# Kernel tuning notes

Hardware: AMD Instinct MI355X
Metric: run time of the kernel (lower is better)

The kernel has to match this reference:

```python
import jax, jax.numpy as jnp
import numpy as np

ALPHA = 0.2     # LeakyReLU negative slope
NEG = -1e9      # mask value for non-edges (matches -1000000000)
N, S, O, H, E = 8192, 128, 64, 4, 262144


def setup_inputs() -> dict:
    key = jax.random.key(0)
    ks = jax.random.split(key, 6)
    x = jax.random.normal(ks[0], (1, N, S), jnp.float32)
    edges = jax.random.randint(ks[1], (2, E), 0, N, dtype=jnp.int64)
    values = jnp.ones((E,), jnp.float32)
    # xavier_normal with gain=1.414
    W_heads = jax.random.normal(ks[2], (H, S, O), jnp.float32) * (1.414 * np.sqrt(2.0 / (S + O)))
    a_heads = jax.random.normal(ks[3], (H, 2 * O), jnp.float32) * (1.414 * np.sqrt(2.0 / (1 + 2 * O)))
    lin_w = jax.random.normal(ks[4], (1, H), jnp.float32) * 0.5
    lin_b = jnp.zeros((1,), jnp.float32)
    return {"x": x, "edges": edges, "values": values, "W_heads": W_heads,
            "a_heads": a_heads, "lin_w": lin_w, "lin_b": lin_b}


def reference(x, edges, values, W_heads, a_heads, lin_w, lin_b):
    b, n, s = x.shape
    Ntot = b * n
    xf = x.reshape(Ntot, s)
    # per-head projection: [H, N, O]
    h = jnp.einsum('ns,hso->hno', xf, W_heads)
    e0, e1 = edges[0], edges[1]
    Od = h.shape[-1]
    # per-edge attention logits for all heads: a . [h_src || h_dst], shape [H, E]
    atts = (jnp.einsum('heo,ho->he', h[:, e0, :], a_heads[:, :Od])
            + jnp.einsum('heo,ho->he', h[:, e1, :], a_heads[:, Od:]))
    atts = jax.nn.leaky_relu(atts, negative_slope=ALPHA)
    # combine heads with a 1-output linear: [E]
    mt = (atts.T @ lin_w.T + lin_b)[:, 0]
    new_values = values * mt
    # scatter to dense NxN (duplicate edges sum, like sparse coo to_dense)
    dense = jnp.zeros((Ntot, Ntot), x.dtype).at[e0, e1].add(new_values)
    a_dense = jnp.zeros((Ntot, Ntot), values.dtype).at[e0, e1].add(values)
    mask = jnp.where(a_dense == 0, NEG, jnp.where(a_dense == 1, 0.0, a_dense))
    # softmax over dim 0, as in the original
    return jax.nn.softmax(dense + mask, axis=0)
```

## Files before the change

kernel.cpp:

```cpp
#include <hip/hip_runtime.h>
#include <math.h>


#define ALPHA 0.2f
constexpr int S = 128;
constexpr int O = 64;
constexpr int H = 4;
constexpr int CAP = 128;
constexpr int RPB = 4;

__global__ void __launch_bounds__(256) k1_scores(
    const float* __restrict__ x, const float* __restrict__ W, const float* __restrict__ a,
    float4* __restrict__ s_src4, float4* __restrict__ s_dst4,
    int* __restrict__ col_cursor, int* __restrict__ row_cursor, int* __restrict__ empty_cnt,
    int N)
{
    __shared__ float wsbuf[2 * H * S];
    int tid = threadIdx.x;
    for (int t = tid; t < 2 * H * S; t += 256) {
        int which = t / (H * S);
        int hs = t % (H * S);
        int h = hs / S, s = hs % S;
        const float* Wr = W + ((size_t)h * S + s) * O;
        const float* av = a + h * 2 * O + which * O;
        float acc = 0.f;
        for (int o = 0; o < O; ++o) acc += Wr[o] * av[o];
        wsbuf[t] = acc;
    }
    __syncthreads();
    int n = blockIdx.x * 256 + tid;
    if (n == 0) empty_cnt[0] = 0;
    if (n >= N) return;
    col_cursor[n] = 0;
    row_cursor[n] = 0;
    const float* wsrc = wsbuf;
    const float* wdst = wsbuf + H * S;
    const float4* xr = (const float4*)(x + (size_t)n * S);
    float accs[H] = {0, 0, 0, 0}, accd[H] = {0, 0, 0, 0};
    for (int i = 0; i < S / 4; ++i) {
        float4 v = xr[i];
#pragma unroll
        for (int h = 0; h < H; ++h) {
            const float* p = wsrc + h * S + i * 4;
            const float* q = wdst + h * S + i * 4;
            accs[h] += v.x * p[0] + v.y * p[1] + v.z * p[2] + v.w * p[3];
            accd[h] += v.x * q[0] + v.y * q[1] + v.z * q[2] + v.w * q[3];
        }
    }
    s_src4[n] = make_float4(accs[0], accs[1], accs[2], accs[3]);
    s_dst4[n] = make_float4(accd[0], accd[1], accd[2], accd[3]);
}

__global__ void __launch_bounds__(256) k2_scatter(
    const int* __restrict__ edges, const float* __restrict__ values,
    const float4* __restrict__ s_src4, const float4* __restrict__ s_dst4,
    const float* __restrict__ lin_w, const float* __restrict__ lin_b,
    int* __restrict__ col_cursor, int* __restrict__ row_cursor,
    int4* __restrict__ col_ent, int* __restrict__ col_r, int N, int E)
{
    int e = blockIdx.x * 256 + threadIdx.x;
    if (e >= E) return;
    int r = edges[e];
    int c = edges[(size_t)E + e];
    if ((unsigned)r >= (unsigned)N || (unsigned)c >= (unsigned)N) return;
    float4 ss = s_src4[r];
    float4 sd = s_dst4[c];
    float att0 = ss.x + sd.x, att1 = ss.y + sd.y, att2 = ss.z + sd.z, att3 = ss.w + sd.w;
    att0 = att0 >= 0.f ? att0 : ALPHA * att0;
    att1 = att1 >= 0.f ? att1 : ALPHA * att1;
    att2 = att2 >= 0.f ? att2 : ALPHA * att2;
    att3 = att3 >= 0.f ? att3 : ALPHA * att3;
    float mt = lin_b[0] + att0 * lin_w[0] + att1 * lin_w[1] + att2 * lin_w[2] + att3 * lin_w[3];
    float av = values[e];
    float nv = av * mt;
    int posc = atomicAdd(&col_cursor[c], 1);
    int posr = atomicAdd(&row_cursor[r], 1);
    if (posc < CAP && posr < CAP) {
        int4 ent;
        ent.x = r;
        ent.y = __float_as_int(nv);
        ent.z = __float_as_int(av);
        ent.w = r * CAP + posr;
        col_ent[(size_t)c * CAP + posc] = ent;
        col_r[(size_t)r * CAP + posr] = c;
    }
}

__global__ void __launch_bounds__(256) k3_softmax(
    const int4* __restrict__ col_ent, const int* __restrict__ col_cursor,
    float* __restrict__ val_r, int* __restrict__ empty_list, int* __restrict__ empty_cnt,
    int N)
{
    int wave = threadIdx.x >> 6, lane = threadIdx.x & 63;
    int j = blockIdx.x * 4 + wave;
    if (j >= N) return;
    int m = col_cursor[j];
    if (m > CAP) m = CAP;
    if (m == 0) {
        if (lane == 0) { int p = atomicAdd(empty_cnt, 1); empty_list[p] = j; }
        return;
    }
    const int4* base = col_ent + (size_t)j * CAP;
    if (m <= 64) {
        bool mine = lane < m;
        int r; float v, av; int link = 0;
        if (mine) {
            int4 ent = base[lane];
            r = ent.x; v = __int_as_float(ent.y); av = __int_as_float(ent.z); link = ent.w;
        } else {
            r = -1 - lane; v = 0.f; av = 0.f;
        }
        float dsum = 0.f, asum = 0.f;
        bool first = true;
        for (int l = 0; l < 64; ++l) {
            int rl = __shfl(r, l);
            float vl = __shfl(v, l);
            float al = __shfl(av, l);
            if (rl == r) {
                dsum += vl; asum += al;
                if (l < lane) first = false;
            }
        }
        float mask = (asum == 1.0f) ? 0.f : asum;
        float val = dsum + mask;
        float lmax = (mine && first) ? val : -INFINITY;
#pragma unroll
        for (int off = 32; off; off >>= 1) lmax = fmaxf(lmax, __shfl_xor(lmax, off));
        float ex = (mine && first) ? expf(val - lmax) : 0.f;
        float lsum = ex;
#pragma unroll
        for (int off = 32; off; off >>= 1) lsum += __shfl_xor(lsum, off);
        float inv = 1.0f / lsum;
        if (mine) val_r[link] = expf(val - lmax) * inv;
    } else {
        float lmax = -INFINITY;
        for (int k = lane; k < m; k += 64) {
            int rk = base[k].x;
            bool first = true;
            float ds = 0.f, as = 0.f;
            for (int l = 0; l < m; ++l) {
                int4 el = base[l];
                if (el.x == rk) {
                    if (l < k) first = false;
                    ds += __int_as_float(el.y);
                    as += __int_as_float(el.z);
                }
            }
            if (first) {
                float mk = (as == 1.0f) ? 0.f : as;
                lmax = fmaxf(lmax, ds + mk);
            }
        }
#pragma unroll
        for (int off = 32; off; off >>= 1) lmax = fmaxf(lmax, __shfl_xor(lmax, off));
        float lsum = 0.f;
        for (int k = lane; k < m; k += 64) {
            int rk = base[k].x;
            bool first = true;
            float ds = 0.f, as = 0.f;
            for (int l = 0; l < m; ++l) {
                int4 el = base[l];
                if (el.x == rk) {
                    if (l < k) first = false;
                    ds += __int_as_float(el.y);
                    as += __int_as_float(el.z);
                }
            }
            if (first) {
                float mk = (as == 1.0f) ? 0.f : as;
                lsum += expf(ds + mk - lmax);
            }
        }
#pragma unroll
        for (int off = 32; off; off >>= 1) lsum += __shfl_xor(lsum, off);
        float inv = 1.0f / lsum;
        for (int k = lane; k < m; k += 64) {
            int rk = base[k].x;
            float ds = 0.f, as = 0.f;
            for (int l = 0; l < m; ++l) {
                int4 el = base[l];
                if (el.x == rk) {
                    ds += __int_as_float(el.y);
                    as += __int_as_float(el.z);
                }
            }
            float mk = (as == 1.0f) ? 0.f : as;
            val_r[base[k].w] = expf(ds + mk - lmax) * inv;
        }
    }
}

__global__ void __launch_bounds__(256) k4_rowwrite(
    const int* __restrict__ col_r, const float* __restrict__ val_r,
    const int* __restrict__ row_cursor, const int* __restrict__ empty_list,
    const int* __restrict__ empty_cnt, float* __restrict__ out, int N)
{
    int t = threadIdx.x;
    const float4 z4 = make_float4(0.f, 0.f, 0.f, 0.f);
    int ec = empty_cnt[0];
    float u = 1.0f / (float)N;
    int n4 = N / 4;
#pragma unroll
    for (int q = 0; q < RPB; ++q) {
        int i = blockIdx.x * RPB + q;
        if (i >= N) return;
        float* orow = out + (size_t)i * N;
        float4* o4 = (float4*)orow;
        for (int k = t; k < n4; k += 256) o4[k] = z4;
        __syncthreads();
        int mr = row_cursor[i];
        if (mr > CAP) mr = CAP;
        const int* cr = col_r + (size_t)i * CAP;
        const float* vr = val_r + (size_t)i * CAP;
        for (int k = t; k < mr; k += 256) orow[cr[k]] = vr[k];
        for (int k = t; k < ec; k += 256) orow[empty_list[k]] = u;
    }
}

extern "C" void kernel_launch(void* const* d_in, const int* in_sizes, int n_in,
                              void* d_out, int out_size, void* d_ws, size_t ws_size,
                              hipStream_t stream) {
    const float* x = (const float*)d_in[0];
    const int* edges = (const int*)d_in[1];
    const float* values = (const float*)d_in[2];
    const float* W = (const float*)d_in[3];
    const float* a = (const float*)d_in[4];
    const float* lin_w = (const float*)d_in[5];
    const float* lin_b = (const float*)d_in[6];
    float* out = (float*)d_out;

    int N = in_sizes[0] / S;
    int E = in_sizes[2];

    char* wsb = (char*)d_ws;
    size_t off = 0;
    auto alloc = [&](size_t bytes) -> void* {
        void* p = wsb + off;
        off += (bytes + 255) & ~(size_t)255;
        return p;
    };
    float4* s_src4 = (float4*)alloc((size_t)N * 16);
    float4* s_dst4 = (float4*)alloc((size_t)N * 16);
    int* col_cursor = (int*)alloc((size_t)N * 4);
    int* row_cursor = (int*)alloc((size_t)N * 4);
    int* empty_cnt = (int*)alloc(256);
    int* empty_list = (int*)alloc((size_t)N * 4);
    int4* col_ent = (int4*)alloc((size_t)N * CAP * 16);
    int* col_r = (int*)alloc((size_t)N * CAP * 4);
    float* val_r = (float*)alloc((size_t)N * CAP * 4);

    k1_scores<<<(N + 255) / 256, 256, 0, stream>>>(x, W, a, s_src4, s_dst4,
                                                   col_cursor, row_cursor, empty_cnt, N);
    k2_scatter<<<(E + 255) / 256, 256, 0, stream>>>(edges, values, s_src4, s_dst4, lin_w, lin_b,
                                                    col_cursor, row_cursor, col_ent, col_r, N, E);
    k3_softmax<<<(N + 3) / 4, 256, 0, stream>>>(col_ent, col_cursor, val_r,
                                                empty_list, empty_cnt, N);
    k4_rowwrite<<<(N + RPB - 1) / RPB, 256, 0, stream>>>(col_r, val_r, row_cursor,
                                                         empty_list, empty_cnt, out, N);
}
```

Baseline: 121.0 us.

## Fuse output zeroing into score kernel and scatter softmax directly to output

```diff
diff --git a/kernel.cpp b/kernel.cpp
--- a/kernel.cpp
+++ b/kernel.cpp
@@ -7,56 +7,61 @@
 constexpr int O = 64;
 constexpr int H = 4;
 constexpr int CAP = 128;
-constexpr int RPB = 4;
-
-__global__ void __launch_bounds__(256) k1_scores(
+
+__global__ void __launch_bounds__(256) k1_zero_scores(
     const float* __restrict__ x, const float* __restrict__ W, const float* __restrict__ a,
     float4* __restrict__ s_src4, float4* __restrict__ s_dst4,
-    int* __restrict__ col_cursor, int* __restrict__ row_cursor, int* __restrict__ empty_cnt,
-    int N)
+    int* __restrict__ col_cursor, float4* __restrict__ out4,
+    int N, size_t n4tot)
 {
     __shared__ float wsbuf[2 * H * S];
     int tid = threadIdx.x;
-    for (int t = tid; t < 2 * H * S; t += 256) {
-        int which = t / (H * S);
-        int hs = t % (H * S);
-        int h = hs / S, s = hs % S;
-        const float* Wr = W + ((size_t)h * S + s) * O;
-        const float* av = a + h * 2 * O + which * O;
-        float acc = 0.f;
-        for (int o = 0; o < O; ++o) acc += Wr[o] * av[o];
-        wsbuf[t] = acc;
-    }
-    __syncthreads();
-    int n = blockIdx.x * 256 + tid;
-    if (n == 0) empty_cnt[0] = 0;
-    if (n >= N) return;
-    col_cursor[n] = 0;
-    row_cursor[n] = 0;
-    const float* wsrc = wsbuf;
-    const float* wdst = wsbuf + H * S;
-    const float4* xr = (const float4*)(x + (size_t)n * S);
-    float accs[H] = {0, 0, 0, 0}, accd[H] = {0, 0, 0, 0};
-    for (int i = 0; i < S / 4; ++i) {
-        float4 v = xr[i];
-#pragma unroll
-        for (int h = 0; h < H; ++h) {
-            const float* p = wsrc + h * S + i * 4;
-            const float* q = wdst + h * S + i * 4;
-            accs[h] += v.x * p[0] + v.y * p[1] + v.z * p[2] + v.w * p[3];
-            accd[h] += v.x * q[0] + v.y * q[1] + v.z * q[2] + v.w * q[3];
-        }
-    }
-    s_src4[n] = make_float4(accs[0], accs[1], accs[2], accs[3]);
-    s_dst4[n] = make_float4(accd[0], accd[1], accd[2], accd[3]);
+    int gt = blockIdx.x * 256 + tid;
+
+    if (blockIdx.x * 256 < N) {
+        for (int t = tid; t < 2 * H * S; t += 256) {
+            int which = t / (H * S);
+            int hs = t % (H * S);
+            int h = hs / S, s = hs % S;
+            const float* Wr = W + ((size_t)h * S + s) * O;
+            const float* av = a + h * 2 * O + which * O;
+            float acc = 0.f;
+            for (int o = 0; o < O; ++o) acc += Wr[o] * av[o];
+            wsbuf[t] = acc;
+        }
+        __syncthreads();
+        int n = gt;
+        if (n < N) {
+            col_cursor[n] = 0;
+            const float* wsrc = wsbuf;
+            const float* wdst = wsbuf + H * S;
+            const float4* xr = (const float4*)(x + (size_t)n * S);
+            float accs[H] = {0, 0, 0, 0}, accd[H] = {0, 0, 0, 0};
+            for (int i = 0; i < S / 4; ++i) {
+                float4 v = xr[i];
+#pragma unroll
+                for (int h = 0; h < H; ++h) {
+                    const float* p = wsrc + h * S + i * 4;
+                    const float* q = wdst + h * S + i * 4;
+                    accs[h] += v.x * p[0] + v.y * p[1] + v.z * p[2] + v.w * p[3];
+                    accd[h] += v.x * q[0] + v.y * q[1] + v.z * q[2] + v.w * q[3];
+                }
+            }
+            s_src4[n] = make_float4(accs[0], accs[1], accs[2], accs[3]);
+            s_dst4[n] = make_float4(accd[0], accd[1], accd[2], accd[3]);
+        }
+    }
+
+    const float4 z4 = make_float4(0.f, 0.f, 0.f, 0.f);
+    size_t GT = (size_t)gridDim.x * 256;
+    for (size_t k = gt; k < n4tot; k += GT) out4[k] = z4;
 }
 
 __global__ void __launch_bounds__(256) k2_scatter(
     const int* __restrict__ edges, const float* __restrict__ values,
     const float4* __restrict__ s_src4, const float4* __restrict__ s_dst4,
     const float* __restrict__ lin_w, const float* __restrict__ lin_b,
-    int* __restrict__ col_cursor, int* __restrict__ row_cursor,
-    int4* __restrict__ col_ent, int* __restrict__ col_r, int N, int E)
+    int* __restrict__ col_cursor, int4* __restrict__ col_ent, int N, int E)
 {
     int e = blockIdx.x * 256 + threadIdx.x;
     if (e >= E) return;
@@ -74,22 +79,19 @@
     float av = values[e];
     float nv = av * mt;
     int posc = atomicAdd(&col_cursor[c], 1);
-    int posr = atomicAdd(&row_cursor[r], 1);
-    if (posc < CAP && posr < CAP) {
+    if (posc < CAP) {
         int4 ent;
         ent.x = r;
         ent.y = __float_as_int(nv);
         ent.z = __float_as_int(av);
-        ent.w = r * CAP + posr;
+        ent.w = 0;
         col_ent[(size_t)c * CAP + posc] = ent;
-        col_r[(size_t)r * CAP + posr] = c;
     }
 }
 
 __global__ void __launch_bounds__(256) k3_softmax(
     const int4* __restrict__ col_ent, const int* __restrict__ col_cursor,
-    float* __restrict__ val_r, int* __restrict__ empty_list, int* __restrict__ empty_cnt,
-    int N)
+    float* __restrict__ out, int N)
 {
     int wave = threadIdx.x >> 6, lane = threadIdx.x & 63;
     int j = blockIdx.x * 4 + wave;
@@ -97,16 +99,17 @@
     int m = col_cursor[j];
     if (m > CAP) m = CAP;
     if (m == 0) {
-        if (lane == 0) { int p = atomicAdd(empty_cnt, 1); empty_list[p] = j; }
+        float u = 1.0f / (float)N;
+        for (int i = lane; i < N; i += 64) out[(size_t)i * N + j] = u;
         return;
     }
     const int4* base = col_ent + (size_t)j * CAP;
     if (m <= 64) {
         bool mine = lane < m;
-        int r; float v, av; int link = 0;
+        int r; float v, av;
         if (mine) {
             int4 ent = base[lane];
-            r = ent.x; v = __int_as_float(ent.y); av = __int_as_float(ent.z); link = ent.w;
+            r = ent.x; v = __int_as_float(ent.y); av = __int_as_float(ent.z);
         } else {
             r = -1 - lane; v = 0.f; av = 0.f;
         }
@@ -131,7 +134,7 @@
 #pragma unroll
         for (int off = 32; off; off >>= 1) lsum += __shfl_xor(lsum, off);
         float inv = 1.0f / lsum;
-        if (mine) val_r[link] = expf(val - lmax) * inv;
+        if (mine) out[(size_t)r * N + j] = expf(val - lmax) * inv;
     } else {
         float lmax = -INFINITY;
         for (int k = lane; k < m; k += 64) {
@@ -185,35 +188,8 @@
                 }
             }
             float mk = (as == 1.0f) ? 0.f : as;
-            val_r[base[k].w] = expf(ds + mk - lmax) * inv;
-        }
-    }
-}
-
-__global__ void __launch_bounds__(256) k4_rowwrite(
-    const int* __restrict__ col_r, const float* __restrict__ val_r,
-    const int* __restrict__ row_cursor, const int* __restrict__ empty_list,
-    const int* __restrict__ empty_cnt, float* __restrict__ out, int N)
-{
-    int t = threadIdx.x;
-    const float4 z4 = make_float4(0.f, 0.f, 0.f, 0.f);
-    int ec = empty_cnt[0];
-    float u = 1.0f / (float)N;
-    int n4 = N / 4;
-#pragma unroll
-    for (int q = 0; q < RPB; ++q) {
-        int i = blockIdx.x * RPB + q;
-        if (i >= N) return;
-        float* orow = out + (size_t)i * N;
-        float4* o4 = (float4*)orow;
-        for (int k = t; k < n4; k += 256) o4[k] = z4;
-        __syncthreads();
-        int mr = row_cursor[i];
-        if (mr > CAP) mr = CAP;
-        const int* cr = col_r + (size_t)i * CAP;
-        const float* vr = val_r + (size_t)i * CAP;
-        for (int k = t; k < mr; k += 256) orow[cr[k]] = vr[k];
-        for (int k = t; k < ec; k += 256) orow[empty_list[k]] = u;
+            out[(size_t)rk * N + j] = expf(ds + mk - lmax) * inv;
+        }
     }
 }
 
@@ -242,19 +218,12 @@
     float4* s_src4 = (float4*)alloc((size_t)N * 16);
     float4* s_dst4 = (float4*)alloc((size_t)N * 16);
     int* col_cursor = (int*)alloc((size_t)N * 4);
-    int* row_cursor = (int*)alloc((size_t)N * 4);
-    int* empty_cnt = (int*)alloc(256);
-    int* empty_list = (int*)alloc((size_t)N * 4);
     int4* col_ent = (int4*)alloc((size_t)N * CAP * 16);
-    int* col_r = (int*)alloc((size_t)N * CAP * 4);
-    float* val_r = (float*)alloc((size_t)N * CAP * 4);
-
-    k1_scores<<<(N + 255) / 256, 256, 0, stream>>>(x, W, a, s_src4, s_dst4,
-                                                   col_cursor, row_cursor, empty_cnt, N);
-    k2_scatter<<<(E + 255) / 256, 256, 0, stream>>>(edges, values, s_src4, s_dst4, lin_w, lin_b,
-                                                    col_cursor, row_cursor, col_ent, col_r, N, E);
-    k3_softmax<<<(N + 3) / 4, 256, 0, stream>>>(col_ent, col_cursor, val_r,
-                                                empty_list, empty_cnt, N);
-    k4_rowwrite<<<(N + RPB - 1) / RPB, 256, 0, stream>>>(col_r, val_r, row_cursor,
-                                                         empty_list, empty_cnt, out, N);
-}
+
+    size_t n4tot = (size_t)N * N / 4;
+    k1_zero_scores<<<2048, 256, 0, stream>>>(x, W, a, s_src4, s_dst4,
+                                             col_cursor, (float4*)out, N, n4tot);
+    k2_scatter<<<(E + 255) / 256, 256, 0, stream>>>(edges, values, s_src4, s_dst4,
+                                                    lin_w, lin_b, col_cursor, col_ent, N, E);
+    k3_softmax<<<(N + 3) / 4, 256, 0, stream>>>(col_ent, col_cursor, out, N);
+}
```

After: 102.7 us. 15.1% less time.
